# Kernel optimization log

Hardware: AMD Instinct MI355X
Metric: run time of the kernel (lower is better)

The kernel has to match this reference:

```python
import jax, jax.numpy as jnp
import numpy as np

# ---- static configuration (matches init_kwargs) ----
D_MODEL = 512
N_HEAD = 16
HEAD_DIM = D_MODEL // N_HEAD
SCALE = HEAD_DIM ** -0.5
SIZE = (64, 64)
WINDOW = (8, 8)
SHIFT = (4, 4)
WS = WINDOW[0] * WINDOW[1]          # tokens per window = 64
NW = (SIZE[0] // WINDOW[0]) * (SIZE[1] // WINDOW[1])  # windows per sample = 64


def _rel_pos_index(window):
    w0, w1 = window
    coords = np.stack(np.meshgrid(np.arange(w0), np.arange(w1), indexing='ij')).reshape(2, -1)
    rel = (coords[:, :, None] - coords[:, None, :]).transpose(1, 2, 0)  # [ws, ws, 2]
    rel[:, :, 0] += w0 - 1
    rel[:, :, 1] += w1 - 1
    rel[:, :, 0] *= 2 * w1 - 1
    return rel.sum(-1)  # [ws, ws] in [0, (2w0-1)(2w1-1))


def _shift_mask(size, window, shift):
    # Swin-style attention mask for shifted windows: 1.0 where tokens belong
    # to different cyclic-shift regions, else 0.0. Shape [nw, ws, ws].
    H, W = size
    w0, w1 = window
    s0, s1 = shift
    img = np.zeros((H, W))
    cnt = 0
    h_slices = (slice(0, -w0), slice(-w0, -s0), slice(-s0, None)) if s0 > 0 else (slice(None),)
    w_slices = (slice(0, -w1), slice(-w1, -s1), slice(-s1, None)) if s1 > 0 else (slice(None),)
    for hs in h_slices:
        for ws_ in w_slices:
            img[hs, ws_] = cnt
            cnt += 1
    win = img.reshape(H // w0, w0, W // w1, w1).transpose(0, 2, 1, 3).reshape(-1, w0 * w1)
    return (win[:, None, :] != win[:, :, None]).astype(np.float32)


REL_IDX = jnp.asarray(_rel_pos_index(WINDOW))              # [ws, ws] int
MASK = jnp.asarray(-100.0 * _shift_mask(SIZE, WINDOW, SHIFT))  # [nw, ws, ws]


def setup_inputs() -> dict:
    key = jax.random.key(0)
    k1, k2, k3, k4 = jax.random.split(key, 4)
    x = jax.random.normal(k1, (8, SIZE[0], SIZE[1], D_MODEL), dtype=jnp.float32)
    qkv_w = jax.random.normal(k2, (3 * D_MODEL, D_MODEL), dtype=jnp.float32) * (D_MODEL ** -0.5)
    qkv_b = jax.random.normal(k3, (3 * D_MODEL,), dtype=jnp.float32) * 0.02
    bias_table = jax.random.normal(k4, ((2 * WINDOW[0] - 1) * (2 * WINDOW[1] - 1), N_HEAD), dtype=jnp.float32) * 0.02
    return {"x": x, "qkv_w": qkv_w, "qkv_b": qkv_b, "bias_table": bias_table}


def reference(x, qkv_w, qkv_b, bias_table):
    n, H, W, c = x.shape
    w0, w1 = WINDOW
    # --- window partition: [n, H, W, c] -> [n*nw, ws, c] ---
    part = x.reshape(n, H // w0, w0, W // w1, w1, c)
    part = part.transpose(0, 1, 3, 2, 4, 5).reshape(n * NW, WS, c)
    # --- qkv projection ---
    qkv = (part @ qkv_w.T + qkv_b).reshape(n * NW, WS, 3, N_HEAD, HEAD_DIM)
    q, k, v = qkv[:, :, 0] * SCALE, qkv[:, :, 1], qkv[:, :, 2]
    # --- scores + relative bias + shift mask + softmax ---
    attn = jnp.einsum('wihd,wjhd->whij', q, k)  # [n*nw, nh, ws, ws]
    bias = bias_table[REL_IDX].transpose(2, 0, 1)  # [nh, ws, ws]
    attn = attn.reshape(n, NW, N_HEAD, WS, WS) + bias[None, None] + MASK[None, :, None]
    attn = jax.nn.softmax(attn, axis=-1).reshape(n * NW, N_HEAD, WS, WS)
    # --- AV + unpartition ---
    out = jnp.einsum('whij,wjhd->wihd', attn, v).reshape(n * NW, WS, c)
    out = out.reshape(n, H // w0, W // w1, w0, w1, c)
    return out.transpose(0, 1, 3, 2, 4, 5).reshape(n, H, W, c)
```

## Files before the change

kernel.cpp:

```cpp
#include <hip/hip_runtime.h>
#include <stdint.h>

typedef unsigned short u16;
typedef __attribute__((ext_vector_type(4))) float floatx4;
typedef __attribute__((ext_vector_type(8))) short bf16x8;

#define MTOK   32768
#define KDIM   512
#define NQKV   1536
#define NWIN   512
#define N_HEAD 16
#define SECSZ  (512 * 16 * 2048)
#define QK_SCALE 0.17677669529663687f

__device__ __forceinline__ u16 f2bf(float f) {
  union { float f; unsigned u; } v; v.f = f;
  unsigned r = v.u + 0x7fffu + ((v.u >> 16) & 1u);
  return (u16)(r >> 16);
}

__device__ __forceinline__ void load_lds16(const void* g, void* l) {
  __builtin_amdgcn_global_load_lds((const __attribute__((address_space(1))) void*)g,
                                   (__attribute__((address_space(3))) void*)l,
                                   16, 0, 0);
}

__global__ __launch_bounds__(256) void convert_xw(const float* __restrict__ x,
                                                  const float* __restrict__ wsrc,
                                                  u16* __restrict__ A,
                                                  u16* __restrict__ Wb) {
  int b = blockIdx.x;
  if (b < 768) {
    int e = (b * 256 + threadIdx.x) * 4;
    const float4 v = *(const float4*)(wsrc + e);
    ushort4 o;
    o.x = f2bf(v.x); o.y = f2bf(v.y); o.z = f2bf(v.z); o.w = f2bf(v.w);
    *(ushort4*)(Wb + e) = o;
  } else {
    int idx = (b - 768) * 256 + threadIdx.x;
    int e = idx * 4;
    int c = e & 511;
    int tg = e >> 9;
    int w = tg >> 6, t = tg & 63;
    int img = w >> 6, wy = (w >> 3) & 7, wx = w & 7;
    int ty = t >> 3, tx = t & 7;
    int y = wy * 8 + ty, xp = wx * 8 + tx;
    const float4 v = *(const float4*)(x + (((img * 64 + y) * 64 + xp) * 512 + c));
    ushort4 o;
    o.x = f2bf(v.x); o.y = f2bf(v.y); o.z = f2bf(v.z); o.w = f2bf(v.w);
    *(ushort4*)(A + e) = o;
  }
}

__global__ __launch_bounds__(256, 4) void gemm_qkv(const u16* __restrict__ A,
                                                   const u16* __restrict__ Wb,
                                                   const float* __restrict__ bias,
                                                   u16* __restrict__ QKV) {
  __shared__ __attribute__((aligned(16))) char smem[18432];
  u16* Ct = (u16*)smem;

  int b = blockIdx.x;
  int xcd = b & 7, slot = b >> 3;
  int mtile = (slot / 12) * 8 + xcd;
  int ntile = slot % 12;

  int tid = threadIdx.x;
  int wv = tid >> 6, lane = tid & 63;
  int il = lane & 15, ch = lane >> 4;
  int wm = (wv & 1) * 64, wn = (wv >> 1) * 64;

  floatx4 acc[4][4];
  floatx4 zacc = {0.f, 0.f, 0.f, 0.f};
#pragma unroll
  for (int m = 0; m < 4; ++m)
#pragma unroll
    for (int n = 0; n < 4; ++n) acc[m][n] = zacc;

  int row0 = tid >> 2;
  int ch4 = (tid & 3) ^ (row0 & 3);
  const u16* Abase = A + (mtile * 128 + row0) * KDIM + ch4 * 8;
  const u16* Bbase = Wb + (ntile * 128 + row0) * KDIM + ch4 * 8;
  char* lAb = smem;
  char* lBb = smem + 8192;
  char* lA0 = lAb + wv * 1024;
  char* lA1 = lAb + 4096 + wv * 1024;
  char* lB0 = lBb + wv * 1024;
  char* lB1 = lBb + 4096 + wv * 1024;

  int sw = il & 3;
  for (int kb = 0; kb < KDIM; kb += 32) {
    __syncthreads();
    load_lds16(Abase + kb, lA0);
    load_lds16(Abase + kb + 64 * KDIM, lA1);
    load_lds16(Bbase + kb, lB0);
    load_lds16(Bbase + kb + 64 * KDIM, lB1);
    __syncthreads();

    bf16x8 af[4], bfr[4];
#pragma unroll
    for (int mt = 0; mt < 4; ++mt)
      af[mt] = *(const bf16x8*)(lAb + (wm + mt * 16 + il) * 64 + (ch ^ sw) * 16);
#pragma unroll
    for (int nt = 0; nt < 4; ++nt)
      bfr[nt] = *(const bf16x8*)(lBb + (wn + nt * 16 + il) * 64 + (ch ^ sw) * 16);
#pragma unroll
    for (int mt = 0; mt < 4; ++mt)
#pragma unroll
      for (int nt = 0; nt < 4; ++nt)
        acc[mt][nt] = __builtin_amdgcn_mfma_f32_16x16x32_bf16(af[mt], bfr[nt], acc[mt][nt], 0, 0, 0);
  }

  __syncthreads();

  int sec = ntile >> 2;
  int h0 = (ntile & 3) * 4;
  int gw0 = mtile * 2;
  u16* dst = QKV + (size_t)sec * SECSZ;
  float sc = (sec == 0) ? QK_SCALE : 1.0f;

  for (int p = 0; p < 2; ++p) {
    if ((wv & 1) == p) {
      if (sec < 2) {
#pragma unroll
        for (int nt = 0; nt < 4; ++nt) {
          float bv = bias[ntile * 128 + wn + nt * 16 + il];
          int cl = wn + nt * 16 + il;
#pragma unroll
          for (int mt = 0; mt < 4; ++mt) {
            int lr = mt * 16 + ch * 4;
#pragma unroll
            for (int r = 0; r < 4; ++r)
              Ct[(lr + r) * 136 + cl] = f2bf((acc[mt][nt][r] + bv) * sc);
          }
        }
      } else {
#pragma unroll
        for (int nt = 0; nt < 4; ++nt) {
          float bv = bias[ntile * 128 + wn + nt * 16 + il];
          int cl = wn + nt * 16 + il;
#pragma unroll
          for (int mt = 0; mt < 4; ++mt) {
            int lr = mt * 16 + ch * 4;
            ushort4 pk;
            pk.x = f2bf(acc[mt][nt][0] + bv);
            pk.y = f2bf(acc[mt][nt][1] + bv);
            pk.z = f2bf(acc[mt][nt][2] + bv);
            pk.w = f2bf(acc[mt][nt][3] + bv);
            *(ushort4*)(Ct + cl * 72 + lr) = pk;
          }
        }
      }
    }
    __syncthreads();

    if (sec < 2) {
      int tl = tid >> 2, dc = tid & 3;
#pragma unroll
      for (int hl = 0; hl < 4; ++hl) {
        uint4 v = *(const uint4*)(smem + tl * 272 + hl * 64 + dc * 16);
        *(uint4*)(dst + ((gw0 + p) * 16 + h0 + hl) * 2048 + tl * 32 + dc * 8) = v;
      }
    } else {
      int c0 = tid >> 3, tq = tid & 7;
#pragma unroll
      for (int hl = 0; hl < 4; ++hl) {
        uint4 v = *(const uint4*)(smem + (hl * 32 + c0) * 144 + tq * 16);
        *(uint4*)(dst + ((gw0 + p) * 16 + h0 + hl) * 2048 + c0 * 64 + tq * 8) = v;
      }
    }
    __syncthreads();
  }
}

__global__ __launch_bounds__(256) void attn(const u16* __restrict__ QKV,
                                            const float* __restrict__ btab,
                                            float* __restrict__ out) {
  __shared__ __attribute__((aligned(16))) u16 Pl[64 * 88];
  __shared__ float sbias[225];

  int bid = blockIdx.x;
  int w = bid >> 4, h = bid & 15;
  int tid = threadIdx.x;
  if (tid < 225) sbias[tid] = btab[tid * 16 + h];

  int lane = tid & 63, wv = tid >> 6;
  int il = lane & 15, ch = lane >> 4;
  const u16* Qb = QKV + (w * 16 + h) * 2048;
  const u16* Kb = Qb + SECSZ;
  const u16* Vt = Qb + 2 * (size_t)SECSZ;

  bf16x8 aq = *(const bf16x8*)(Qb + (wv * 16 + il) * 32 + ch * 8);
  floatx4 zacc = {0.f, 0.f, 0.f, 0.f};
  floatx4 s[4];
#pragma unroll
  for (int jt = 0; jt < 4; ++jt) {
    bf16x8 bk = *(const bf16x8*)(Kb + (jt * 16 + il) * 32 + ch * 8);
    s[jt] = __builtin_amdgcn_mfma_f32_16x16x32_bf16(aq, bk, zacc, 0, 0, 0);
  }

  __syncthreads();

  int winidx = w & 63;
  int wy = winidx >> 3, wx = winidx & 7;
  float val[4][4];
#pragma unroll
  for (int r = 0; r < 4; ++r) {
    int i = wv * 16 + ch * 4 + r;
    int ty = i >> 3, tx = i & 7;
    int ry = (wy == 7) ? (ty < 4 ? 1 : 2) : 0;
    int rx = (wx == 7) ? (tx < 4 ? 1 : 2) : 0;
    int li = ry * 3 + rx;
#pragma unroll
    for (int jt = 0; jt < 4; ++jt) {
      int j = jt * 16 + il;
      int sy = j >> 3, sx = j & 7;
      int rjy = (wy == 7) ? (sy < 4 ? 1 : 2) : 0;
      int rjx = (wx == 7) ? (sx < 4 ? 1 : 2) : 0;
      float v = s[jt][r] + sbias[(ty - sy + 7) * 15 + (tx - sx + 7)];
      if (li != (rjy * 3 + rjx)) v -= 100.0f;
      val[r][jt] = v;
    }
  }

#pragma unroll
  for (int r = 0; r < 4; ++r) {
    float m = fmaxf(fmaxf(val[r][0], val[r][1]), fmaxf(val[r][2], val[r][3]));
    m = fmaxf(m, __shfl_xor(m, 1, 64));
    m = fmaxf(m, __shfl_xor(m, 2, 64));
    m = fmaxf(m, __shfl_xor(m, 4, 64));
    m = fmaxf(m, __shfl_xor(m, 8, 64));
    float sum = 0.f;
#pragma unroll
    for (int jt = 0; jt < 4; ++jt) { val[r][jt] = __expf(val[r][jt] - m); sum += val[r][jt]; }
    sum += __shfl_xor(sum, 1, 64);
    sum += __shfl_xor(sum, 2, 64);
    sum += __shfl_xor(sum, 4, 64);
    sum += __shfl_xor(sum, 8, 64);
    float inv = 1.0f / sum;
    int i = wv * 16 + ch * 4 + r;
#pragma unroll
    for (int jt = 0; jt < 4; ++jt)
      Pl[i * 88 + jt * 16 + il] = f2bf(val[r][jt] * inv);
  }

  __syncthreads();

  floatx4 o0 = zacc, o1 = zacc;
#pragma unroll
  for (int kk = 0; kk < 2; ++kk) {
    bf16x8 ap  = *(const bf16x8*)((const u16*)Pl + (wv * 16 + il) * 88 + kk * 32 + ch * 8);
    bf16x8 bv0 = *(const bf16x8*)(Vt + il * 64 + kk * 32 + ch * 8);
    bf16x8 bv1 = *(const bf16x8*)(Vt + (16 + il) * 64 + kk * 32 + ch * 8);
    o0 = __builtin_amdgcn_mfma_f32_16x16x32_bf16(ap, bv0, o0, 0, 0, 0);
    o1 = __builtin_amdgcn_mfma_f32_16x16x32_bf16(ap, bv1, o1, 0, 0, 0);
  }

  int img = w >> 6;
#pragma unroll
  for (int r = 0; r < 4; ++r) {
    int i = wv * 16 + ch * 4 + r;
    int ty = i >> 3, tx = i & 7;
    int y = wy * 8 + ty, xp = wx * 8 + tx;
    float* op = out + ((img * 64 + y) * 64 + xp) * 512 + h * 32;
    op[il] = o0[r];
    op[16 + il] = o1[r];
  }
}

extern "C" void kernel_launch(void* const* d_in, const int* in_sizes, int n_in,
                              void* d_out, int out_size, void* d_ws, size_t ws_size,
                              hipStream_t stream) {
  const float* x      = (const float*)d_in[0];
  const float* qkv_w  = (const float*)d_in[1];
  const float* qkv_b  = (const float*)d_in[2];
  const float* btab   = (const float*)d_in[3];
  float* out = (float*)d_out;

  char* ws = (char*)d_ws;
  u16* A   = (u16*)ws;
  u16* Wb  = (u16*)(ws + (size_t)MTOK * KDIM * 2);
  u16* QKV = (u16*)(ws + (size_t)MTOK * KDIM * 2 + (size_t)NQKV * KDIM * 2);

  convert_xw<<<dim3(17152), dim3(256), 0, stream>>>(x, qkv_w, A, Wb);
  gemm_qkv<<<dim3(3072), dim3(256), 0, stream>>>(A, Wb, qkv_b, QKV);
  attn<<<dim3(NWIN * N_HEAD), dim3(256), 0, stream>>>(QKV, btab, out);
}
```

Measured before the change: 225.4 us.

## Enlarge QKV GEMM tiles to 256x256 with double-buffered async LDS pipeline

Rewrites the QKV projection GEMM to use 256x256 output tiles per 512-thread block instead of 128x128 per 256-thread block, with K chunks of 64 double-buffered in 128KB of LDS and global-to-LDS loads for the next chunk issued between MFMA groups, plus setprio around the MFMAs. The larger tiles are meant to cut global and LDS traffic per FLOP and hide load latency behind compute. The epilogue is also reworked for the bigger tile. In exchange it uses heavy LDS and more registers per block (8x4 accumulators), which lowers occupancy to one or two blocks per CU. It also depends on hand-placed waitcnt and barrier ordering for correctness.

```diff
diff --git a/kernel.cpp b/kernel.cpp
--- a/kernel.cpp
+++ b/kernel.cpp
@@ -52,123 +52,158 @@
   }
 }
 
-__global__ __launch_bounds__(256, 4) void gemm_qkv(const u16* __restrict__ A,
+__global__ __launch_bounds__(512, 2) void gemm_qkv(const u16* __restrict__ A,
                                                    const u16* __restrict__ Wb,
                                                    const float* __restrict__ bias,
                                                    u16* __restrict__ QKV) {
-  __shared__ __attribute__((aligned(16))) char smem[18432];
-  u16* Ct = (u16*)smem;
+  __shared__ __attribute__((aligned(16))) char smem[131072];
 
   int b = blockIdx.x;
-  int xcd = b & 7, slot = b >> 3;
-  int mtile = (slot / 12) * 8 + xcd;
-  int ntile = slot % 12;
-
-  int tid = threadIdx.x;
-  int wv = tid >> 6, lane = tid & 63;
-  int il = lane & 15, ch = lane >> 4;
-  int wm = (wv & 1) * 64, wn = (wv >> 1) * 64;
-
-  floatx4 acc[4][4];
+  int lin = (b & 7) * 96 + (b >> 3);
+  int mtile = lin / 6;
+  int ntile = lin % 6;
+
+  const int tid = threadIdx.x;
+  const int wv = tid >> 6, lane = tid & 63;
+  const int il = lane & 15, ch = lane >> 4;
+  const int wm = wv >> 2, wn = wv & 3;
+
+  const int srow = tid >> 3;
+  const int csw  = (tid & 7) ^ (srow & 7);
+  const u16* gA = A  + (size_t)(mtile * 256 + srow) * KDIM + csw * 8;
+  const u16* gB = Wb + (size_t)(ntile * 256 + srow) * KDIM + csw * 8;
+
+#define STG_A(t_, c_) load_lds16(gA + (t_) * 64 + (c_) * 32768, smem + (((t_) & 1) * 65536) + (c_) * 8192 + wv * 1024)
+#define STG_B(t_, c_) load_lds16(gB + (t_) * 64 + (c_) * 32768, smem + (((t_) & 1) * 65536) + 32768 + (c_) * 8192 + wv * 1024)
+
+  const int abrow = (wm * 128 + il) * 128;
+  const int bbrow = 32768 + (wn * 64 + il) * 128;
+  const int sw0 = ((0 + ch) ^ (il & 7)) << 4;
+  const int sw1 = ((4 + ch) ^ (il & 7)) << 4;
+
+  floatx4 acc[8][4];
   floatx4 zacc = {0.f, 0.f, 0.f, 0.f};
 #pragma unroll
-  for (int m = 0; m < 4; ++m)
+  for (int m = 0; m < 8; ++m)
 #pragma unroll
     for (int n = 0; n < 4; ++n) acc[m][n] = zacc;
 
-  int row0 = tid >> 2;
-  int ch4 = (tid & 3) ^ (row0 & 3);
-  const u16* Abase = A + (mtile * 128 + row0) * KDIM + ch4 * 8;
-  const u16* Bbase = Wb + (ntile * 128 + row0) * KDIM + ch4 * 8;
-  char* lAb = smem;
-  char* lBb = smem + 8192;
-  char* lA0 = lAb + wv * 1024;
-  char* lA1 = lAb + 4096 + wv * 1024;
-  char* lB0 = lBb + wv * 1024;
-  char* lB1 = lBb + 4096 + wv * 1024;
-
-  int sw = il & 3;
-  for (int kb = 0; kb < KDIM; kb += 32) {
-    __syncthreads();
-    load_lds16(Abase + kb, lA0);
-    load_lds16(Abase + kb + 64 * KDIM, lA1);
-    load_lds16(Bbase + kb, lB0);
-    load_lds16(Bbase + kb + 64 * KDIM, lB1);
-    __syncthreads();
-
-    bf16x8 af[4], bfr[4];
-#pragma unroll
-    for (int mt = 0; mt < 4; ++mt)
-      af[mt] = *(const bf16x8*)(lAb + (wm + mt * 16 + il) * 64 + (ch ^ sw) * 16);
-#pragma unroll
-    for (int nt = 0; nt < 4; ++nt)
-      bfr[nt] = *(const bf16x8*)(lBb + (wn + nt * 16 + il) * 64 + (ch ^ sw) * 16);
-#pragma unroll
-    for (int mt = 0; mt < 4; ++mt)
-#pragma unroll
-      for (int nt = 0; nt < 4; ++nt)
-        acc[mt][nt] = __builtin_amdgcn_mfma_f32_16x16x32_bf16(af[mt], bfr[nt], acc[mt][nt], 0, 0, 0);
-  }
-
-  __syncthreads();
-
-  int sec = ntile >> 2;
-  int h0 = (ntile & 3) * 4;
-  int gw0 = mtile * 2;
+  STG_A(0, 0); STG_A(0, 1); STG_A(0, 2); STG_A(0, 3);
+  STG_B(0, 0); STG_B(0, 1); STG_B(0, 2); STG_B(0, 3);
+  STG_B(1, 0); STG_B(1, 1); STG_B(1, 2); STG_B(1, 3);
+
+#pragma unroll
+  for (int t = 0; t < 8; ++t) {
+    const int sb = (t & 1) * 65536;
+    if (t == 7) asm volatile("s_waitcnt vmcnt(0)" ::: "memory");
+    else        asm volatile("s_waitcnt vmcnt(4)" ::: "memory");
+    __builtin_amdgcn_s_barrier();
+
+    bf16x8 bf[4][2];
+#pragma unroll
+    for (int nt = 0; nt < 4; ++nt) {
+      bf[nt][0] = *(const bf16x8*)(smem + sb + bbrow + nt * 2048 + sw0);
+      bf[nt][1] = *(const bf16x8*)(smem + sb + bbrow + nt * 2048 + sw1);
+    }
+
+#pragma unroll
+    for (int p = 0; p < 4; ++p) {
+      const char* ab = smem + sb + abrow + p * 4096;
+      bf16x8 a00 = *(const bf16x8*)(ab + sw0);
+      bf16x8 a01 = *(const bf16x8*)(ab + sw1);
+      bf16x8 a10 = *(const bf16x8*)(ab + 2048 + sw0);
+      bf16x8 a11 = *(const bf16x8*)(ab + 2048 + sw1);
+
+      if (p < 2) {
+        if (t < 7) { STG_A(t + 1, p * 2); STG_A(t + 1, p * 2 + 1); }
+      } else {
+        if (t < 6) { STG_B(t + 2, p * 2 - 4); STG_B(t + 2, p * 2 - 3); }
+      }
+
+      __builtin_amdgcn_s_barrier();
+      asm volatile("s_waitcnt lgkmcnt(0)" ::: "memory");
+      __builtin_amdgcn_s_setprio(1);
+#pragma unroll
+      for (int nt = 0; nt < 4; ++nt) {
+        acc[2 * p][nt]     = __builtin_amdgcn_mfma_f32_16x16x32_bf16(a00, bf[nt][0], acc[2 * p][nt], 0, 0, 0);
+        acc[2 * p][nt]     = __builtin_amdgcn_mfma_f32_16x16x32_bf16(a01, bf[nt][1], acc[2 * p][nt], 0, 0, 0);
+        acc[2 * p + 1][nt] = __builtin_amdgcn_mfma_f32_16x16x32_bf16(a10, bf[nt][0], acc[2 * p + 1][nt], 0, 0, 0);
+        acc[2 * p + 1][nt] = __builtin_amdgcn_mfma_f32_16x16x32_bf16(a11, bf[nt][1], acc[2 * p + 1][nt], 0, 0, 0);
+      }
+      __builtin_amdgcn_s_setprio(0);
+      __builtin_amdgcn_s_barrier();
+    }
+  }
+#undef STG_A
+#undef STG_B
+
+  const int sec = ntile >> 1;
+  const int h0v = (ntile & 1) * 8;
+  const int gw0 = mtile * 4;
   u16* dst = QKV + (size_t)sec * SECSZ;
-  float sc = (sec == 0) ? QK_SCALE : 1.0f;
+  const float sc = (sec == 0) ? QK_SCALE : 1.0f;
+
+  float bv[4];
+#pragma unroll
+  for (int nt = 0; nt < 4; ++nt) bv[nt] = bias[ntile * 256 + wn * 64 + nt * 16 + il];
+
+  u16* Lt = (u16*)smem;
 
   for (int p = 0; p < 2; ++p) {
-    if ((wv & 1) == p) {
+    if (wm == p) {
       if (sec < 2) {
 #pragma unroll
-        for (int nt = 0; nt < 4; ++nt) {
-          float bv = bias[ntile * 128 + wn + nt * 16 + il];
-          int cl = wn + nt * 16 + il;
-#pragma unroll
-          for (int mt = 0; mt < 4; ++mt) {
-            int lr = mt * 16 + ch * 4;
+        for (int mt = 0; mt < 8; ++mt) {
+          int tl = mt * 16 + ch * 4;
+#pragma unroll
+          for (int nt = 0; nt < 4; ++nt) {
+            int cc = wn * 64 + nt * 16 + il;
 #pragma unroll
             for (int r = 0; r < 4; ++r)
-              Ct[(lr + r) * 136 + cl] = f2bf((acc[mt][nt][r] + bv) * sc);
+              Lt[(tl + r) * 264 + cc] = f2bf((acc[mt][nt][r] + bv[nt]) * sc);
           }
         }
       } else {
 #pragma unroll
-        for (int nt = 0; nt < 4; ++nt) {
-          float bv = bias[ntile * 128 + wn + nt * 16 + il];
-          int cl = wn + nt * 16 + il;
-#pragma unroll
-          for (int mt = 0; mt < 4; ++mt) {
-            int lr = mt * 16 + ch * 4;
+        for (int mt = 0; mt < 8; ++mt) {
+          int tl = mt * 16 + ch * 4;
+#pragma unroll
+          for (int nt = 0; nt < 4; ++nt) {
+            int cc = wn * 64 + nt * 16 + il;
             ushort4 pk;
-            pk.x = f2bf(acc[mt][nt][0] + bv);
-            pk.y = f2bf(acc[mt][nt][1] + bv);
-            pk.z = f2bf(acc[mt][nt][2] + bv);
-            pk.w = f2bf(acc[mt][nt][3] + bv);
-            *(ushort4*)(Ct + cl * 72 + lr) = pk;
+            pk.x = f2bf(acc[mt][nt][0] + bv[nt]);
+            pk.y = f2bf(acc[mt][nt][1] + bv[nt]);
+            pk.z = f2bf(acc[mt][nt][2] + bv[nt]);
+            pk.w = f2bf(acc[mt][nt][3] + bv[nt]);
+            *(ushort4*)(Lt + cc * 136 + tl) = pk;
           }
         }
       }
     }
-    __syncthreads();
+    asm volatile("s_waitcnt lgkmcnt(0)" ::: "memory");
+    __builtin_amdgcn_s_barrier();
 
     if (sec < 2) {
-      int tl = tid >> 2, dc = tid & 3;
-#pragma unroll
-      for (int hl = 0; hl < 4; ++hl) {
-        uint4 v = *(const uint4*)(smem + tl * 272 + hl * 64 + dc * 16);
-        *(uint4*)(dst + ((gw0 + p) * 16 + h0 + hl) * 2048 + tl * 32 + dc * 8) = v;
+#pragma unroll
+      for (int i = 0; i < 2; ++i) {
+        int task = tid + i * 512;
+        int tl = task >> 3, hh = task & 7;
+        const uint4* srcp = (const uint4*)(Lt + tl * 264 + hh * 32);
+        uint4 v0 = srcp[0], v1 = srcp[1], v2 = srcp[2], v3 = srcp[3];
+        int w = gw0 + 2 * p + (tl >> 6);
+        uint4* o = (uint4*)(dst + (size_t)(w * 16 + h0v + hh) * 2048 + (tl & 63) * 32);
+        o[0] = v0; o[1] = v1; o[2] = v2; o[3] = v3;
       }
     } else {
-      int c0 = tid >> 3, tq = tid & 7;
-#pragma unroll
-      for (int hl = 0; hl < 4; ++hl) {
-        uint4 v = *(const uint4*)(smem + (hl * 32 + c0) * 144 + tq * 16);
-        *(uint4*)(dst + ((gw0 + p) * 16 + h0 + hl) * 2048 + c0 * 64 + tq * 8) = v;
-      }
-    }
-    __syncthreads();
+      int c = tid >> 1, wl = tid & 1;
+      const uint4* srcp = (const uint4*)(Lt + c * 136 + wl * 64);
+      int w = gw0 + 2 * p + wl;
+      uint4* o = (uint4*)(dst + (size_t)(w * 16 + h0v + (c >> 5)) * 2048 + (c & 31) * 64);
+#pragma unroll
+      for (int i = 0; i < 8; ++i) o[i] = srcp[i];
+    }
+    asm volatile("s_waitcnt lgkmcnt(0)" ::: "memory");
+    __builtin_amdgcn_s_barrier();
   }
 }
 
@@ -282,6 +317,6 @@
   u16* QKV = (u16*)(ws + (size_t)MTOK * KDIM * 2 + (size_t)NQKV * KDIM * 2);
 
   convert_xw<<<dim3(17152), dim3(256), 0, stream>>>(x, qkv_w, A, Wb);
-  gemm_qkv<<<dim3(3072), dim3(256), 0, stream>>>(A, Wb, qkv_b, QKV);
+  gemm_qkv<<<dim3(768), dim3(512), 0, stream>>>(A, Wb, qkv_b, QKV);
   attn<<<dim3(NWIN * N_HEAD), dim3(256), 0, stream>>>(QKV, btab, out);
 }
```

New measurement: 236.5 us. 1.05x slower.

## Precompute bias+mask tables per window class and reswizzle GEMM LDS layout

Applied to the files above, without the earlier changes.

The convert kernel now also builds a dense 64x64 bias-plus-shift-mask table for each of the 4 window classes and 16 heads. The attention kernel reads these values directly instead of staging bias in shared memory, computing region indices and branching per element, which also removes a block barrier. Separately, the GEMM's LDS staging changes to an 8-way XOR swizzle over 128-byte rows to reduce bank conflicts on fragment reads. The cost is extra workspace and about 1 MB of table reads from global memory or cache in the attention kernel.

```diff
diff --git a/kernel.cpp b/kernel.cpp
--- a/kernel.cpp
+++ b/kernel.cpp
@@ -27,8 +27,10 @@
 
 __global__ __launch_bounds__(256) void convert_xw(const float* __restrict__ x,
                                                   const float* __restrict__ wsrc,
+                                                  const float* __restrict__ btab,
                                                   u16* __restrict__ A,
-                                                  u16* __restrict__ Wb) {
+                                                  u16* __restrict__ Wb,
+                                                  float* __restrict__ tbl) {
   int b = blockIdx.x;
   if (b < 768) {
     int e = (b * 256 + threadIdx.x) * 4;
@@ -36,7 +38,7 @@
     ushort4 o;
     o.x = f2bf(v.x); o.y = f2bf(v.y); o.z = f2bf(v.z); o.w = f2bf(v.w);
     *(ushort4*)(Wb + e) = o;
-  } else {
+  } else if (b < 17152) {
     int idx = (b - 768) * 256 + threadIdx.x;
     int e = idx * 4;
     int c = e & 511;
@@ -49,6 +51,24 @@
     ushort4 o;
     o.x = f2bf(v.x); o.y = f2bf(v.y); o.z = f2bf(v.z); o.w = f2bf(v.w);
     *(ushort4*)(A + e) = o;
+  } else {
+    int q = b - 17152;
+    int cls = q >> 4, hh = q & 15;
+    int ey = cls >> 1, ex = cls & 1;
+    float* To = tbl + (q << 12);
+#pragma unroll
+    for (int e = 0; e < 16; ++e) {
+      int idx = e * 256 + threadIdx.x;
+      int i = idx >> 6, j = idx & 63;
+      int ty = i >> 3, tx = i & 7, sy = j >> 3, sx = j & 7;
+      int ry = ey ? (ty < 4 ? 1 : 2) : 0;
+      int rx = ex ? (tx < 4 ? 1 : 2) : 0;
+      int qy = ey ? (sy < 4 ? 1 : 2) : 0;
+      int qx = ex ? (sx < 4 ? 1 : 2) : 0;
+      float v = btab[((ty - sy + 7) * 15 + (tx - sx + 7)) * 16 + hh];
+      if (ry * 3 + rx != qy * 3 + qx) v -= 100.0f;
+      To[idx] = v;
+    }
   }
 }
 
@@ -76,8 +96,9 @@
 #pragma unroll
     for (int n = 0; n < 4; ++n) acc[m][n] = zacc;
 
-  int row0 = tid >> 2;
-  int ch4 = (tid & 3) ^ (row0 & 3);
+  int s8   = (tid & 7) ^ ((tid >> 3) & 7);
+  int row0 = ((tid >> 3) << 1) + (s8 >> 2);
+  int ch4  = s8 & 3;
   const u16* Abase = A + (mtile * 128 + row0) * KDIM + ch4 * 8;
   const u16* Bbase = Wb + (ntile * 128 + row0) * KDIM + ch4 * 8;
   char* lAb = smem;
@@ -87,7 +108,11 @@
   char* lB0 = lBb + wv * 1024;
   char* lB1 = lBb + 4096 + wv * 1024;
 
-  int sw = il & 3;
+  int aslot = ((il & 1) * 4 + ch) ^ ((il >> 1) & 7);
+  int fbase = (il >> 1) * 128 + aslot * 16;
+  int awoff = (wv & 1) * 4096;
+  int bwoff = (wv >> 1) * 4096;
+
   for (int kb = 0; kb < KDIM; kb += 32) {
     __syncthreads();
     load_lds16(Abase + kb, lA0);
@@ -99,10 +124,10 @@
     bf16x8 af[4], bfr[4];
 #pragma unroll
     for (int mt = 0; mt < 4; ++mt)
-      af[mt] = *(const bf16x8*)(lAb + (wm + mt * 16 + il) * 64 + (ch ^ sw) * 16);
+      af[mt] = *(const bf16x8*)(lAb + awoff + fbase + mt * 1024);
 #pragma unroll
     for (int nt = 0; nt < 4; ++nt)
-      bfr[nt] = *(const bf16x8*)(lBb + (wn + nt * 16 + il) * 64 + (ch ^ sw) * 16);
+      bfr[nt] = *(const bf16x8*)(lBb + bwoff + fbase + nt * 1024);
 #pragma unroll
     for (int mt = 0; mt < 4; ++mt)
 #pragma unroll
@@ -173,15 +198,13 @@
 }
 
 __global__ __launch_bounds__(256) void attn(const u16* __restrict__ QKV,
-                                            const float* __restrict__ btab,
+                                            const float* __restrict__ tbl,
                                             float* __restrict__ out) {
   __shared__ __attribute__((aligned(16))) u16 Pl[64 * 88];
-  __shared__ float sbias[225];
 
   int bid = blockIdx.x;
   int w = bid >> 4, h = bid & 15;
   int tid = threadIdx.x;
-  if (tid < 225) sbias[tid] = btab[tid * 16 + h];
 
   int lane = tid & 63, wv = tid >> 6;
   int il = lane & 15, ch = lane >> 4;
@@ -198,28 +221,18 @@
     s[jt] = __builtin_amdgcn_mfma_f32_16x16x32_bf16(aq, bk, zacc, 0, 0, 0);
   }
 
-  __syncthreads();
-
   int winidx = w & 63;
   int wy = winidx >> 3, wx = winidx & 7;
+  int cls = ((wy == 7) ? 2 : 0) | ((wx == 7) ? 1 : 0);
+  const float* T = tbl + (((cls << 4) | h) << 12);
+
   float val[4][4];
 #pragma unroll
   for (int r = 0; r < 4; ++r) {
     int i = wv * 16 + ch * 4 + r;
-    int ty = i >> 3, tx = i & 7;
-    int ry = (wy == 7) ? (ty < 4 ? 1 : 2) : 0;
-    int rx = (wx == 7) ? (tx < 4 ? 1 : 2) : 0;
-    int li = ry * 3 + rx;
-#pragma unroll
-    for (int jt = 0; jt < 4; ++jt) {
-      int j = jt * 16 + il;
-      int sy = j >> 3, sx = j & 7;
-      int rjy = (wy == 7) ? (sy < 4 ? 1 : 2) : 0;
-      int rjx = (wx == 7) ? (sx < 4 ? 1 : 2) : 0;
-      float v = s[jt][r] + sbias[(ty - sy + 7) * 15 + (tx - sx + 7)];
-      if (li != (rjy * 3 + rjx)) v -= 100.0f;
-      val[r][jt] = v;
-    }
+#pragma unroll
+    for (int jt = 0; jt < 4; ++jt)
+      val[r][jt] = s[jt][r] + T[i * 64 + jt * 16 + il];
   }
 
 #pragma unroll
@@ -277,11 +290,13 @@
   float* out = (float*)d_out;
 
   char* ws = (char*)d_ws;
-  u16* A   = (u16*)ws;
-  u16* Wb  = (u16*)(ws + (size_t)MTOK * KDIM * 2);
-  u16* QKV = (u16*)(ws + (size_t)MTOK * KDIM * 2 + (size_t)NQKV * KDIM * 2);
-
-  convert_xw<<<dim3(17152), dim3(256), 0, stream>>>(x, qkv_w, A, Wb);
+  u16* A    = (u16*)ws;
+  u16* Wb   = (u16*)(ws + (size_t)MTOK * KDIM * 2);
+  u16* QKV  = (u16*)(ws + (size_t)MTOK * KDIM * 2 + (size_t)NQKV * KDIM * 2);
+  float* tbl = (float*)(ws + (size_t)MTOK * KDIM * 2 + (size_t)NQKV * KDIM * 2
+                           + 3 * (size_t)SECSZ * 2);
+
+  convert_xw<<<dim3(17216), dim3(256), 0, stream>>>(x, qkv_w, btab, A, Wb, tbl);
   gemm_qkv<<<dim3(3072), dim3(256), 0, stream>>>(A, Wb, qkv_b, QKV);
-  attn<<<dim3(NWIN * N_HEAD), dim3(256), 0, stream>>>(QKV, btab, out);
-}
+  attn<<<dim3(NWIN * N_HEAD), dim3(256), 0, stream>>>(QKV, tbl, out);
+}
```

After: 226.9 us. No clear change (+0.7%).
